# Kernel optimization log

Measured on AMD Instinct MI355X. Metric: run time of the kernel, lower is better.

Reference implementation:

```python
import jax, jax.numpy as jnp
import numpy as np

N, E, B = 50000, 800000, 512
IN, H, OUT = 128, 64, 32
BN_EPS = 1e-5


def setup_inputs() -> dict:
    key = jax.random.key(0)
    ks = jax.random.split(key, 32)
    inp = {}
    inp["x"] = jax.random.normal(ks[0], (N, IN), dtype=jnp.float32)
    inp["edge_index"] = jax.random.randint(ks[1], (2, E), 0, N, dtype=jnp.int64)
    inp["batch"] = jnp.sort(jax.random.randint(ks[2], (N,), 0, B, dtype=jnp.int64))
    inp["batch_size"] = B
    # GINConv MLP params: Linear(cin,H) -> BN(H) -> ReLU -> Linear(H,H)
    cins = [IN, H, H]
    ki = 3
    for i, cin in enumerate(cins):
        inp[f"c{i}_W1"] = jax.random.normal(ks[ki], (cin, H), dtype=jnp.float32) / np.sqrt(cin); ki += 1
        inp[f"c{i}_b1"] = jnp.zeros((H,), jnp.float32)
        inp[f"c{i}_g1"] = jnp.ones((H,), jnp.float32)
        inp[f"c{i}_bt1"] = jnp.zeros((H,), jnp.float32)
        inp[f"c{i}_W2"] = jax.random.normal(ks[ki], (H, H), dtype=jnp.float32) / np.sqrt(H); ki += 1
        inp[f"c{i}_b2"] = jnp.zeros((H,), jnp.float32)
    # final MLP (norm=None): Linear(H,H) -> ReLU -> [dropout, eval: identity] -> Linear(H,OUT)
    inp["f_W1"] = jax.random.normal(ks[ki], (H, H), dtype=jnp.float32) / np.sqrt(H); ki += 1
    inp["f_b1"] = jnp.zeros((H,), jnp.float32)
    inp["f_W2"] = jax.random.normal(ks[ki], (H, OUT), dtype=jnp.float32) / np.sqrt(H)
    inp["f_b2"] = jnp.zeros((OUT,), jnp.float32)
    return inp


def _bn(h, g, bt):
    # BatchNorm1d, training-mode statistics (biased variance), eps=1e-5
    mean = h.mean(axis=0)
    var = ((h - mean) ** 2).mean(axis=0)
    return g * (h - mean) * jax.lax.rsqrt(var + BN_EPS) + bt


def _gin_conv(x, src, dst, W1, b1, g1, bt1, W2, b2):
    # sum-aggregate neighbor features: agg[i] = sum_{(j->i)} x[j]
    agg = jax.ops.segment_sum(x[src], dst, num_segments=N)  # [N,H_in]
    h = x + agg  # (1+eps)*x + agg, eps=0
    h = jax.nn.relu(_bn(h @ W1 + b1, g1, bt1))
    return h @ W2 + b2


def reference(x, edge_index, batch, batch_size,
              c0_W1, c0_b1, c0_g1, c0_bt1, c0_W2, c0_b2,
              c1_W1, c1_b1, c1_g1, c1_bt1, c1_W2, c1_b2,
              c2_W1, c2_b1, c2_g1, c2_bt1, c2_W2, c2_b2,
              f_W1, f_b1, f_W2, f_b2):
    src, dst = edge_index[0], edge_index[1]
    convs = [(c0_W1, c0_b1, c0_g1, c0_bt1, c0_W2, c0_b2),
             (c1_W1, c1_b1, c1_g1, c1_bt1, c1_W2, c1_b2),
             (c2_W1, c2_b1, c2_g1, c2_bt1, c2_W2, c2_b2)]
    for p in convs:
        x = jax.nn.relu(_gin_conv(x, src, dst, *p))
    # global_add_pool over graph ids
    pooled = jax.ops.segment_sum(x, batch, num_segments=batch_size)  # [B,H]
    h = jax.nn.relu(pooled @ f_W1 + f_b1)  # dropout=0.5 skipped (eval mode)
    return h @ f_W2 + f_b2  # [B,OUT]
```

## Files before the change

kernel.cpp:

```cpp
#include <hip/hip_runtime.h>
#include <hip/hip_fp16.h>

#define NN 50000
#define EE 800000
#define BB 512
#define DIN 128
#define HH 64
#define DOUT 32
#define BN_EPS 1e-5f
#define SCAN_BLOCKS 196
#define NGRP 6250
#define GATHER_GRID 1024

template <int CIN>
__global__ __launch_bounds__(256) void proj_kernel(const float* __restrict__ X,
                                                   const float* __restrict__ W,
                                                   __half2* __restrict__ Qh)
{
    __shared__ float sW[CIN * 64];
    __shared__ float sX[16 * CIN];
    const int tid = threadIdx.x;
    const int row0 = blockIdx.x * 16;

    for (int i = tid; i < CIN * 16; i += 256)
        ((float4*)sW)[i] = ((const float4*)W)[i];
    const float* Xb = X + (size_t)row0 * CIN;
    for (int i = tid; i < 16 * CIN / 4; i += 256)
        ((float4*)sX)[i] = ((const float4*)Xb)[i];
    __syncthreads();

    const int col2 = tid & 31;
    const int rg   = tid >> 5;
    float2 acc0 = {0.f, 0.f};
    float2 acc1 = {0.f, 0.f};
    const float* x0p = &sX[(rg * 2 + 0) * CIN];
    const float* x1p = &sX[(rg * 2 + 1) * CIN];
#pragma unroll 4
    for (int k = 0; k < CIN; ++k) {
        const float2 w = *(const float2*)&sW[k * 64 + col2 * 2];
        const float x0 = x0p[k];
        const float x1 = x1p[k];
        acc0.x = fmaf(x0, w.x, acc0.x);
        acc0.y = fmaf(x0, w.y, acc0.y);
        acc1.x = fmaf(x1, w.x, acc1.x);
        acc1.y = fmaf(x1, w.y, acc1.y);
    }
    const int r0 = row0 + rg * 2;
    Qh[(size_t)(r0 + 0) * 32 + col2] = __floats2half2_rn(acc0.x, acc0.y);
    Qh[(size_t)(r0 + 1) * 32 + col2] = __floats2half2_rn(acc1.x, acc1.y);
}

__global__ __launch_bounds__(256) void hist_rank_kernel(const int* __restrict__ dst,
                                                        int* __restrict__ deg,
                                                        int* __restrict__ rank)
{
    const int e = blockIdx.x * 256 + threadIdx.x;
    rank[e] = atomicAdd(&deg[dst[e]], 1);
}

__global__ __launch_bounds__(256) void scanA_kernel(const int* __restrict__ deg,
                                                    int* __restrict__ offs,
                                                    int* __restrict__ blockSums)
{
    __shared__ int s[256];
    const int t = threadIdx.x;
    const int i = blockIdx.x * 256 + t;
    const int v = (i < NN) ? deg[i] : 0;
    s[t] = v;
    __syncthreads();
    for (int off = 1; off < 256; off <<= 1) {
        const int a = (t >= off) ? s[t - off] : 0;
        __syncthreads();
        s[t] += a;
        __syncthreads();
    }
    if (i < NN) offs[i] = s[t] - v;
    if (t == 255) blockSums[blockIdx.x] = s[255];
}

__global__ __launch_bounds__(256) void scanB_kernel(const int* __restrict__ blockSums,
                                                    int* __restrict__ blockOff)
{
    __shared__ int s[256];
    const int t = threadIdx.x;
    const int v = (t < SCAN_BLOCKS) ? blockSums[t] : 0;
    s[t] = v;
    __syncthreads();
    for (int off = 1; off < 256; off <<= 1) {
        const int a = (t >= off) ? s[t - off] : 0;
        __syncthreads();
        s[t] += a;
        __syncthreads();
    }
    if (t < SCAN_BLOCKS) blockOff[t] = s[t] - v;
}

__global__ __launch_bounds__(256) void scanC_kernel(int* __restrict__ offs,
                                                    const int* __restrict__ blockOff,
                                                    float* __restrict__ statsbuf,
                                                    float* __restrict__ pooled)
{
    const int i = blockIdx.x * 256 + threadIdx.x;
    if (i < NN) offs[i] += blockOff[blockIdx.x];
    if (i == 0) offs[NN] = EE;
    if (i < 384) statsbuf[i] = 0.f;
    if (i < BB * 64) pooled[i] = 0.f;
}

__global__ __launch_bounds__(256) void scatter_kernel(const int* __restrict__ src,
                                                      const int* __restrict__ dst,
                                                      const int* __restrict__ rank,
                                                      const int* __restrict__ offs,
                                                      int* __restrict__ srcSorted)
{
    const int e = blockIdx.x * 256 + threadIdx.x;
    const int pos = offs[dst[e]] + rank[e];
    srcSorted[pos] = src[e];
}

__global__ __launch_bounds__(256) void gather_kernel(const __half2* __restrict__ Qh,
                                                     const int* __restrict__ offs,
                                                     const int* __restrict__ srcSorted,
                                                     const float* __restrict__ b1,
                                                     float* __restrict__ Z,
                                                     float* __restrict__ sums,
                                                     float* __restrict__ sumsq)
{
    const int tid  = threadIdx.x;
    const int half = tid & 31;
    const int sel8 = tid >> 5;
    const float2 bb = ((const float2*)b1)[half];
    float2 s  = {0.f, 0.f};
    float2 ss = {0.f, 0.f};

    for (int g = blockIdx.x; g < NGRP; g += GATHER_GRID) {
        const int node = g * 8 + sel8;
        const int o0 = offs[node];
        const int o1 = offs[node + 1];
        float2 acc = __half22float2(Qh[(size_t)node * 32 + half]);
        acc.x += bb.x;
        acc.y += bb.y;
        int j = o0;
        for (; j + 4 <= o1; j += 4) {
            const int i0 = srcSorted[j + 0];
            const int i1 = srcSorted[j + 1];
            const int i2 = srcSorted[j + 2];
            const int i3 = srcSorted[j + 3];
            const float2 a0 = __half22float2(Qh[(size_t)i0 * 32 + half]);
            const float2 a1 = __half22float2(Qh[(size_t)i1 * 32 + half]);
            const float2 a2 = __half22float2(Qh[(size_t)i2 * 32 + half]);
            const float2 a3 = __half22float2(Qh[(size_t)i3 * 32 + half]);
            acc.x += a0.x + a1.x + a2.x + a3.x;
            acc.y += a0.y + a1.y + a2.y + a3.y;
        }
        for (; j < o1; ++j) {
            const float2 a = __half22float2(Qh[(size_t)srcSorted[j] * 32 + half]);
            acc.x += a.x;
            acc.y += a.y;
        }
        ((float2*)Z)[(size_t)node * 32 + half] = acc;
        s.x += acc.x; s.y += acc.y;
        ss.x += acc.x * acc.x; ss.y += acc.y * acc.y;
    }

    __shared__ float red[8][32][4];
    red[sel8][half][0] = s.x;
    red[sel8][half][1] = s.y;
    red[sel8][half][2] = ss.x;
    red[sel8][half][3] = ss.y;
    __syncthreads();
    if (tid < 32) {
        float a0 = 0.f, a1 = 0.f, a2 = 0.f, a3 = 0.f;
#pragma unroll
        for (int r = 0; r < 8; ++r) {
            a0 += red[r][tid][0];
            a1 += red[r][tid][1];
            a2 += red[r][tid][2];
            a3 += red[r][tid][3];
        }
        atomicAdd(&sums[2 * tid + 0], a0);
        atomicAdd(&sums[2 * tid + 1], a1);
        atomicAdd(&sumsq[2 * tid + 0], a2);
        atomicAdd(&sumsq[2 * tid + 1], a3);
    }
}

template <bool POOL>
__global__ __launch_bounds__(256) void gemm2_kernel(const float* __restrict__ Z,
                                                    const float* __restrict__ sums,
                                                    const float* __restrict__ sumsq,
                                                    const float* __restrict__ g1,
                                                    const float* __restrict__ bt1,
                                                    const float* __restrict__ W2,
                                                    const float* __restrict__ b2,
                                                    const int* __restrict__ batch,
                                                    float* __restrict__ out)
{
    __shared__ float sW[64 * 64];
    __shared__ float sH[16 * 64];
    __shared__ float sScale[64];
    __shared__ float sShift[64];
    const int tid = threadIdx.x;
    const int row0 = blockIdx.x * 16;

    if (tid < 64) {
        const float inv_n = 1.0f / (float)NN;
        const float mean = sums[tid] * inv_n;
        const float var = fmaxf(sumsq[tid] * inv_n - mean * mean, 0.f);
        const float sc = g1[tid] * rsqrtf(var + BN_EPS);
        sScale[tid] = sc;
        sShift[tid] = bt1[tid] - mean * sc;
    }
    for (int i = tid; i < 64 * 16; i += 256)
        ((float4*)sW)[i] = ((const float4*)W2)[i];
    __syncthreads();

    const float4* Zb = (const float4*)(Z + (size_t)row0 * 64);
    {
        const int i = tid;
        const float4 z = Zb[i];
        const int c4 = i & 15;
        const float4 sc = ((const float4*)sScale)[c4];
        const float4 sh = ((const float4*)sShift)[c4];
        float4 h;
        h.x = fmaxf(fmaf(z.x, sc.x, sh.x), 0.f);
        h.y = fmaxf(fmaf(z.y, sc.y, sh.y), 0.f);
        h.z = fmaxf(fmaf(z.z, sc.z, sh.z), 0.f);
        h.w = fmaxf(fmaf(z.w, sc.w, sh.w), 0.f);
        ((float4*)sH)[i] = h;
    }
    __syncthreads();

    const int col = tid & 63;
    const int r0  = tid >> 6;
    const float bc = b2[col];
    float acc[4] = {bc, bc, bc, bc};
    for (int k = 0; k < 64; k += 4) {
        const float w0 = sW[(k + 0) * 64 + col];
        const float w1 = sW[(k + 1) * 64 + col];
        const float w2 = sW[(k + 2) * 64 + col];
        const float w3 = sW[(k + 3) * 64 + col];
#pragma unroll
        for (int rr = 0; rr < 4; ++rr) {
            const float4 hv = *(const float4*)&sH[(r0 + rr * 4) * 64 + k];
            acc[rr] = fmaf(hv.x, w0, acc[rr]);
            acc[rr] = fmaf(hv.y, w1, acc[rr]);
            acc[rr] = fmaf(hv.z, w2, acc[rr]);
            acc[rr] = fmaf(hv.w, w3, acc[rr]);
        }
    }
#pragma unroll
    for (int rr = 0; rr < 4; ++rr) {
        const int row = row0 + r0 + rr * 4;
        const float v = fmaxf(acc[rr], 0.f);
        if (POOL) {
            atomicAdd(&out[(size_t)batch[row] * 64 + col], v);
        } else {
            out[(size_t)row * 64 + col] = v;
        }
    }
}

__global__ __launch_bounds__(256) void final_mlp(const float* __restrict__ P,
                                                 const float* __restrict__ W1,
                                                 const float* __restrict__ b1,
                                                 const float* __restrict__ W2,
                                                 const float* __restrict__ b2,
                                                 float* __restrict__ out)
{
    __shared__ float sW1[64 * 64];
    __shared__ float sW2[64 * 32];
    __shared__ float sH[4 * 64];
    const int tid = threadIdx.x;
    const int row0 = blockIdx.x * 4;

    for (int i = tid; i < 1024; i += 256) ((float4*)sW1)[i] = ((const float4*)W1)[i];
    for (int i = tid; i < 512; i += 256) ((float4*)sW2)[i] = ((const float4*)W2)[i];
    __syncthreads();

    const int col = tid & 63;
    const int r = tid >> 6;
    float acc = b1[col];
    const float* prow = P + (size_t)(row0 + r) * 64;
    for (int k = 0; k < 64; ++k) acc = fmaf(prow[k], sW1[k * 64 + col], acc);
    sH[r * 64 + col] = fmaxf(acc, 0.f);
    __syncthreads();

    if (tid < 128) {
        const int c = tid & 31;
        const int r2 = tid >> 5;
        float a2 = b2[c];
        for (int k = 0; k < 64; ++k) a2 = fmaf(sH[r2 * 64 + k], sW2[k * 32 + c], a2);
        out[(size_t)(row0 + r2) * 32 + c] = a2;
    }
}

extern "C" void kernel_launch(void* const* d_in, const int* in_sizes, int n_in,
                              void* d_out, int out_size, void* d_ws, size_t ws_size,
                              hipStream_t stream)
{
    const float* x   = (const float*)d_in[0];
    const int* ei    = (const int*)d_in[1];
    const int* batch = (const int*)d_in[2];
    const float* cW1[3] = {(const float*)d_in[4],  (const float*)d_in[10], (const float*)d_in[16]};
    const float* cb1[3] = {(const float*)d_in[5],  (const float*)d_in[11], (const float*)d_in[17]};
    const float* cg1[3] = {(const float*)d_in[6],  (const float*)d_in[12], (const float*)d_in[18]};
    const float* cbt[3] = {(const float*)d_in[7],  (const float*)d_in[13], (const float*)d_in[19]};
    const float* cW2[3] = {(const float*)d_in[8],  (const float*)d_in[14], (const float*)d_in[20]};
    const float* cb2[3] = {(const float*)d_in[9],  (const float*)d_in[15], (const float*)d_in[21]};
    const float* fW1 = (const float*)d_in[22];
    const float* fb1 = (const float*)d_in[23];
    const float* fW2 = (const float*)d_in[24];
    const float* fb2 = (const float*)d_in[25];
    float* out = (float*)d_out;

    float* bufX     = (float*)d_ws;
    __half2* Qh     = (__half2*)(bufX + (size_t)NN * 64);
    float* pooled   = (float*)(Qh + (size_t)NN * 32);
    float* statsbuf = pooled + (size_t)BB * 64;
    int* deg        = (int*)(statsbuf + 384);
    int* offs       = deg + NN;
    int* rank       = offs + (NN + 1);
    int* blockSums  = rank + EE;
    int* blockOff   = blockSums + 256;
    int* srcSorted  = blockOff + 256;

    const int* esrc = ei;
    const int* edst = ei + EE;

    const int gemm_blocks = NN / 16;
    const int edge_blocks = EE / 256;

    hipMemsetAsync(deg, 0, NN * sizeof(int), stream);
    hist_rank_kernel<<<edge_blocks, 256, 0, stream>>>(edst, deg, rank);
    scanA_kernel<<<SCAN_BLOCKS, 256, 0, stream>>>(deg, offs, blockSums);
    scanB_kernel<<<1, 256, 0, stream>>>(blockSums, blockOff);
    scanC_kernel<<<SCAN_BLOCKS, 256, 0, stream>>>(offs, blockOff, statsbuf, pooled);
    scatter_kernel<<<edge_blocks, 256, 0, stream>>>(esrc, edst, rank, offs, srcSorted);

    for (int layer = 0; layer < 3; ++layer) {
        float* sums  = statsbuf + layer * 128;
        float* sumsq = sums + 64;

        if (layer == 0)
            proj_kernel<DIN><<<gemm_blocks, 256, 0, stream>>>(x, cW1[0], Qh);
        else
            proj_kernel<HH><<<gemm_blocks, 256, 0, stream>>>(bufX, cW1[layer], Qh);

        gather_kernel<<<GATHER_GRID, 256, 0, stream>>>(Qh, offs, srcSorted, cb1[layer],
                                                       bufX, sums, sumsq);

        if (layer < 2) {
            gemm2_kernel<false><<<gemm_blocks, 256, 0, stream>>>(bufX, sums, sumsq, cg1[layer],
                                                                 cbt[layer], cW2[layer], cb2[layer],
                                                                 nullptr, bufX);
        } else {
            gemm2_kernel<true><<<gemm_blocks, 256, 0, stream>>>(bufX, sums, sumsq, cg1[layer],
                                                                cbt[layer], cW2[layer], cb2[layer],
                                                                batch, pooled);
        }
    }

    final_mlp<<<BB / 4, 256, 0, stream>>>(pooled, fW1, fb1, fW2, fb2, out);
}
```

Measured before the change: 402.8 us.

## Use wave-per-node edge-parallel gather and 16-bit edge index arrays

```diff
diff --git a/kernel.cpp b/kernel.cpp
--- a/kernel.cpp
+++ b/kernel.cpp
@@ -9,8 +9,7 @@
 #define DOUT 32
 #define BN_EPS 1e-5f
 #define SCAN_BLOCKS 196
-#define NGRP 6250
-#define GATHER_GRID 1024
+#define GATHER_BLOCKS 1024
 
 template <int CIN>
 __global__ __launch_bounds__(256) void proj_kernel(const float* __restrict__ X,
@@ -52,10 +51,10 @@
 
 __global__ __launch_bounds__(256) void hist_rank_kernel(const int* __restrict__ dst,
                                                         int* __restrict__ deg,
-                                                        int* __restrict__ rank)
+                                                        unsigned short* __restrict__ rank)
 {
     const int e = blockIdx.x * 256 + threadIdx.x;
-    rank[e] = atomicAdd(&deg[dst[e]], 1);
+    rank[e] = (unsigned short)atomicAdd(&deg[dst[e]], 1);
 }
 
 __global__ __launch_bounds__(256) void scanA_kernel(const int* __restrict__ deg,
@@ -109,79 +108,101 @@
 
 __global__ __launch_bounds__(256) void scatter_kernel(const int* __restrict__ src,
                                                       const int* __restrict__ dst,
-                                                      const int* __restrict__ rank,
+                                                      const unsigned short* __restrict__ rank,
                                                       const int* __restrict__ offs,
-                                                      int* __restrict__ srcSorted)
+                                                      unsigned short* __restrict__ srcSorted)
 {
     const int e = blockIdx.x * 256 + threadIdx.x;
-    const int pos = offs[dst[e]] + rank[e];
-    srcSorted[pos] = src[e];
+    const int pos = offs[dst[e]] + (int)rank[e];
+    srcSorted[pos] = (unsigned short)src[e];
 }
 
 __global__ __launch_bounds__(256) void gather_kernel(const __half2* __restrict__ Qh,
                                                      const int* __restrict__ offs,
-                                                     const int* __restrict__ srcSorted,
+                                                     const unsigned short* __restrict__ srcSorted,
                                                      const float* __restrict__ b1,
                                                      float* __restrict__ Z,
                                                      float* __restrict__ sums,
                                                      float* __restrict__ sumsq)
 {
     const int tid  = threadIdx.x;
-    const int half = tid & 31;
-    const int sel8 = tid >> 5;
-    const float2 bb = ((const float2*)b1)[half];
-    float2 s  = {0.f, 0.f};
-    float2 ss = {0.f, 0.f};
-
-    for (int g = blockIdx.x; g < NGRP; g += GATHER_GRID) {
-        const int node = g * 8 + sel8;
+    const int lane = tid & 63;
+    const int wid  = tid >> 6;
+    const int colq = lane & 15;
+    const int grp  = lane >> 4;
+    const uint2* Qr = (const uint2*)Qh;
+    const float4 bb = ((const float4*)b1)[colq];
+
+    float sa0 = 0.f, sa1 = 0.f, sa2 = 0.f, sa3 = 0.f;
+    float ta0 = 0.f, ta1 = 0.f, ta2 = 0.f, ta3 = 0.f;
+
+    for (int node = blockIdx.x * 4 + wid; node < NN; node += GATHER_BLOCKS * 4) {
         const int o0 = offs[node];
         const int o1 = offs[node + 1];
-        float2 acc = __half22float2(Qh[(size_t)node * 32 + half]);
-        acc.x += bb.x;
-        acc.y += bb.y;
+        float a0 = 0.f, a1 = 0.f, a2 = 0.f, a3 = 0.f;
         int j = o0;
+        for (; j + 16 <= o1; j += 16) {
+            const int e0 = srcSorted[j + grp];
+            const int e1 = srcSorted[j + 4 + grp];
+            const int e2 = srcSorted[j + 8 + grp];
+            const int e3 = srcSorted[j + 12 + grp];
+            const uint2 r0 = Qr[(size_t)e0 * 16 + colq];
+            const uint2 r1 = Qr[(size_t)e1 * 16 + colq];
+            const uint2 r2 = Qr[(size_t)e2 * 16 + colq];
+            const uint2 r3 = Qr[(size_t)e3 * 16 + colq];
+            float2 p;
+            p = __half22float2(*(const __half2*)&r0.x); a0 += p.x; a1 += p.y;
+            p = __half22float2(*(const __half2*)&r0.y); a2 += p.x; a3 += p.y;
+            p = __half22float2(*(const __half2*)&r1.x); a0 += p.x; a1 += p.y;
+            p = __half22float2(*(const __half2*)&r1.y); a2 += p.x; a3 += p.y;
+            p = __half22float2(*(const __half2*)&r2.x); a0 += p.x; a1 += p.y;
+            p = __half22float2(*(const __half2*)&r2.y); a2 += p.x; a3 += p.y;
+            p = __half22float2(*(const __half2*)&r3.x); a0 += p.x; a1 += p.y;
+            p = __half22float2(*(const __half2*)&r3.y); a2 += p.x; a3 += p.y;
+        }
         for (; j + 4 <= o1; j += 4) {
-            const int i0 = srcSorted[j + 0];
-            const int i1 = srcSorted[j + 1];
-            const int i2 = srcSorted[j + 2];
-            const int i3 = srcSorted[j + 3];
-            const float2 a0 = __half22float2(Qh[(size_t)i0 * 32 + half]);
-            const float2 a1 = __half22float2(Qh[(size_t)i1 * 32 + half]);
-            const float2 a2 = __half22float2(Qh[(size_t)i2 * 32 + half]);
-            const float2 a3 = __half22float2(Qh[(size_t)i3 * 32 + half]);
-            acc.x += a0.x + a1.x + a2.x + a3.x;
-            acc.y += a0.y + a1.y + a2.y + a3.y;
-        }
-        for (; j < o1; ++j) {
-            const float2 a = __half22float2(Qh[(size_t)srcSorted[j] * 32 + half]);
-            acc.x += a.x;
-            acc.y += a.y;
-        }
-        ((float2*)Z)[(size_t)node * 32 + half] = acc;
-        s.x += acc.x; s.y += acc.y;
-        ss.x += acc.x * acc.x; ss.y += acc.y * acc.y;
-    }
-
-    __shared__ float red[8][32][4];
-    red[sel8][half][0] = s.x;
-    red[sel8][half][1] = s.y;
-    red[sel8][half][2] = ss.x;
-    red[sel8][half][3] = ss.y;
-    __syncthreads();
-    if (tid < 32) {
-        float a0 = 0.f, a1 = 0.f, a2 = 0.f, a3 = 0.f;
-#pragma unroll
-        for (int r = 0; r < 8; ++r) {
-            a0 += red[r][tid][0];
-            a1 += red[r][tid][1];
-            a2 += red[r][tid][2];
-            a3 += red[r][tid][3];
-        }
-        atomicAdd(&sums[2 * tid + 0], a0);
-        atomicAdd(&sums[2 * tid + 1], a1);
-        atomicAdd(&sumsq[2 * tid + 0], a2);
-        atomicAdd(&sumsq[2 * tid + 1], a3);
+            const int e0 = srcSorted[j + grp];
+            const uint2 r0 = Qr[(size_t)e0 * 16 + colq];
+            float2 p;
+            p = __half22float2(*(const __half2*)&r0.x); a0 += p.x; a1 += p.y;
+            p = __half22float2(*(const __half2*)&r0.y); a2 += p.x; a3 += p.y;
+        }
+        if (grp < o1 - j) {
+            const int e0 = srcSorted[j + grp];
+            const uint2 r0 = Qr[(size_t)e0 * 16 + colq];
+            float2 p;
+            p = __half22float2(*(const __half2*)&r0.x); a0 += p.x; a1 += p.y;
+            p = __half22float2(*(const __half2*)&r0.y); a2 += p.x; a3 += p.y;
+        }
+        a0 += __shfl_xor(a0, 16); a1 += __shfl_xor(a1, 16);
+        a2 += __shfl_xor(a2, 16); a3 += __shfl_xor(a3, 16);
+        a0 += __shfl_xor(a0, 32); a1 += __shfl_xor(a1, 32);
+        a2 += __shfl_xor(a2, 32); a3 += __shfl_xor(a3, 32);
+        if (grp == 0) {
+            const uint2 sr = Qr[(size_t)node * 16 + colq];
+            float2 p;
+            p = __half22float2(*(const __half2*)&sr.x); a0 += p.x + bb.x; a1 += p.y + bb.y;
+            p = __half22float2(*(const __half2*)&sr.y); a2 += p.x + bb.z; a3 += p.y + bb.w;
+            float4 zv = {a0, a1, a2, a3};
+            ((float4*)Z)[(size_t)node * 16 + colq] = zv;
+            sa0 += a0; sa1 += a1; sa2 += a2; sa3 += a3;
+            ta0 += a0 * a0; ta1 += a1 * a1; ta2 += a2 * a2; ta3 += a3 * a3;
+        }
+    }
+
+    __shared__ float red[4][16][8];
+    if (grp == 0) {
+        float* rp = red[wid][colq];
+        rp[0] = sa0; rp[1] = sa1; rp[2] = sa2; rp[3] = sa3;
+        rp[4] = ta0; rp[5] = ta1; rp[6] = ta2; rp[7] = ta3;
+    }
+    __syncthreads();
+    if (tid < 128) {
+        const int cq = tid >> 3;
+        const int k  = tid & 7;
+        const float v = red[0][cq][k] + red[1][cq][k] + red[2][cq][k] + red[3][cq][k];
+        float* dstp = (k < 4) ? &sums[cq * 4 + k] : &sumsq[cq * 4 + (k - 4)];
+        atomicAdd(dstp, v);
     }
 }
 
@@ -320,10 +341,10 @@
     float* statsbuf = pooled + (size_t)BB * 64;
     int* deg        = (int*)(statsbuf + 384);
     int* offs       = deg + NN;
-    int* rank       = offs + (NN + 1);
-    int* blockSums  = rank + EE;
+    int* blockSums  = offs + (NN + 1);
     int* blockOff   = blockSums + 256;
-    int* srcSorted  = blockOff + 256;
+    unsigned short* rank      = (unsigned short*)(blockOff + 256);
+    unsigned short* srcSorted = rank + EE;
 
     const int* esrc = ei;
     const int* edst = ei + EE;
@@ -347,8 +368,8 @@
         else
             proj_kernel<HH><<<gemm_blocks, 256, 0, stream>>>(bufX, cW1[layer], Qh);
 
-        gather_kernel<<<GATHER_GRID, 256, 0, stream>>>(Qh, offs, srcSorted, cb1[layer],
-                                                       bufX, sums, sumsq);
+        gather_kernel<<<GATHER_BLOCKS, 256, 0, stream>>>(Qh, offs, srcSorted, cb1[layer],
+                                                         bufX, sums, sumsq);
 
         if (layer < 2) {
             gemm2_kernel<false><<<gemm_blocks, 256, 0, stream>>>(bufX, sums, sumsq, cg1[layer],
```

Result: faster. 341.8 us (-15.1%).
